# Performance work log

Hardware: AMD Instinct MI355X
Metric: run time of the kernel (lower is better)

## Reference

```python
import jax, jax.numpy as jnp
import numpy as np

N, E, F, D, H, HID, OUT, G = 25000, 400000, 128, 16, 64, 128, 32, 64

def silu(v):
    return v * jax.nn.sigmoid(v)

def setup_inputs() -> dict:
    key = jax.random.key(0)
    ks = jax.random.split(key, 32)
    inp = {
        'x': jax.random.normal(ks[0], (N, F), jnp.float32),
        'pos': jax.random.normal(ks[1], (N, 3), jnp.float32),
        'edge_attr': jax.random.normal(ks[2], (E, D), jnp.float32),
        'edge_index': jax.random.randint(ks[3], (2, E), 0, N, jnp.int64),
        'batch': jnp.sort(jax.random.randint(ks[4], (N,), 0, G, jnp.int64)),
    }
    def lin(k, fan_in, fan_out):
        return jax.random.normal(k, (fan_in, fan_out), jnp.float32) / np.sqrt(fan_in)
    i = 5
    for l, in_c in enumerate([F, HID]):
        cat = 2 * in_c + D + 1
        inp[f'l{l}_mlp_w'] = lin(ks[i], cat, H); i += 1
        inp[f'l{l}_edge_w'] = lin(ks[i], H, H); i += 1
        inp[f'l{l}_edge_b'] = jnp.zeros((H,), jnp.float32)
        inp[f'l{l}_coord_w'] = lin(ks[i], H, 1); i += 1
        inp[f'l{l}_coord_b'] = jnp.zeros((1,), jnp.float32)
        inp[f'l{l}_node_w1'] = lin(ks[i], in_c + H, H); i += 1
        inp[f'l{l}_node_b1'] = jnp.zeros((H,), jnp.float32)
        inp[f'l{l}_node_w2'] = lin(ks[i], H, HID); i += 1
        inp[f'l{l}_node_b2'] = jnp.zeros((HID,), jnp.float32)
    inp['out_w1'] = lin(ks[i], HID, HID); i += 1
    inp['out_b1'] = jnp.zeros((HID,), jnp.float32)
    inp['out_w2'] = lin(ks[i], HID, OUT); i += 1
    inp['out_b2'] = jnp.zeros((OUT,), jnp.float32)
    return inp

def egnn_layer(x, pos, src, dst, edge_attr, mlp_w, edge_w, edge_b, coord_w, coord_b, nw1, nb1, nw2, nb2):
    # PyG flow source_to_target: i = dst (edge_index[1]), j = src (edge_index[0])
    diff = pos[dst] - pos[src]                    # (E,3)
    radial = jnp.sum(diff * diff, axis=1, keepdims=True)  # (E,1)
    cat = jnp.concatenate([x[dst], x[src], edge_attr, radial], axis=1)
    h = silu(cat @ mlp_w)                         # (E,H)
    e_ij = silu(h @ edge_w + edge_b)              # (E,H)
    coord_update = diff * silu(e_ij @ coord_w + coord_b)  # (E,3)
    e_agg = jax.ops.segment_sum(e_ij, dst, num_segments=N)          # sum reduce
    cu_sum = jax.ops.segment_sum(coord_update, dst, num_segments=N)
    deg = jax.ops.segment_sum(jnp.ones((E, 1), x.dtype), dst, num_segments=N)
    cu_mean = cu_sum / jnp.maximum(deg, 1.0)      # mean reduce, 0 for isolated nodes
    h_node = silu(jnp.concatenate([x, e_agg], axis=1) @ nw1 + nb1) @ nw2 + nb2
    return h_node, pos + cu_mean

def reference(x, pos, edge_attr, edge_index, batch,
              l0_mlp_w, l0_edge_w, l0_edge_b, l0_coord_w, l0_coord_b, l0_node_w1, l0_node_b1, l0_node_w2, l0_node_b2,
              l1_mlp_w, l1_edge_w, l1_edge_b, l1_coord_w, l1_coord_b, l1_node_w1, l1_node_b1, l1_node_w2, l1_node_b2,
              out_w1, out_b1, out_w2, out_b2):
    src, dst = edge_index[0], edge_index[1]
    x, pos = egnn_layer(x, pos, src, dst, edge_attr, l0_mlp_w, l0_edge_w, l0_edge_b, l0_coord_w, l0_coord_b, l0_node_w1, l0_node_b1, l0_node_w2, l0_node_b2)
    x, pos = egnn_layer(x, pos, src, dst, edge_attr, l1_mlp_w, l1_edge_w, l1_edge_b, l1_coord_w, l1_coord_b, l1_node_w1, l1_node_b1, l1_node_w2, l1_node_b2)
    # graph mean pooling over batch assignment
    g_sum = jax.ops.segment_sum(x, batch, num_segments=G)
    g_cnt = jax.ops.segment_sum(jnp.ones((N, 1), x.dtype), batch, num_segments=G)
    g = g_sum / jnp.maximum(g_cnt, 1.0)           # (G, HID)
    g = jax.nn.relu(g)
    return jax.nn.relu(g @ out_w1 + out_b1) @ out_w2 + out_b2  # (G, OUT)
```

## Files before the change

### kernel.cpp

```cpp
#include <hip/hip_runtime.h>
#include <math.h>

#define NN 25000
#define EE 400000
#define FF 128
#define DD 16
#define HH 64
#define HIDC 128
#define OUTC 32
#define GG 64
#define NODEBLK 782
#define SCATBLK 1563
#define NTILES 1563

#define EDGEBLK 2048
#define EW_Q 3
#define EW_R 424
#define HS_STRIDE 68

#define WQ_NW1 0
#define WQ_NW2 24576
#define WQ_WN  40960
#define WQ_EW  73728
#define WQ_W3  77824
#define WQ_LAYER 81920

typedef __attribute__((ext_vector_type(8))) short short8;
typedef __attribute__((ext_vector_type(8))) unsigned short u16x8;
typedef __attribute__((ext_vector_type(4))) float f32x4;

union S8 { short8 v; unsigned short u[8]; };
union U8 { u16x8 v; unsigned short u[8]; };

__device__ __forceinline__ float silu_f(float v) {
    return v / (1.f + __expf(-v));
}

__device__ __forceinline__ unsigned short f2bf_rne(float f) {
  unsigned u = __float_as_uint(f);
  unsigned r = u + 0x7fffu + ((u >> 16) & 1u);
  return (unsigned short)(r >> 16);
}
__device__ __forceinline__ float bfbits2f(unsigned short b) {
  return __uint_as_float(((unsigned)b) << 16);
}

__device__ __forceinline__ void split8(const float* hv, S8& hi, S8& lo) {
#pragma unroll
  for (int j = 0; j < 8; ++j) {
    const unsigned short hb = (unsigned short)(__float_as_uint(hv[j]) >> 16);
    hi.u[j] = hb;
    lo.u[j] = f2bf_rne(hv[j] - bfbits2f(hb));
  }
}

__device__ __forceinline__ f32x4 mfma3(const S8& ah, const S8& al,
                                       const S8& bh, const S8& bl, f32x4 c) {
  c = __builtin_amdgcn_mfma_f32_16x16x32_bf16(ah.v, bh.v, c, 0, 0, 0);
  c = __builtin_amdgcn_mfma_f32_16x16x32_bf16(al.v, bh.v, c, 0, 0, 0);
  c = __builtin_amdgcn_mfma_f32_16x16x32_bf16(ah.v, bl.v, c, 0, 0, 0);
  return c;
}

__device__ __forceinline__ void prepSplit(unsigned short* dst, const float* __restrict__ W,
                                          int ldw, int k0, int n0, int q, int m, int lane) {
  S8 hi, lo;
#pragma unroll
  for (int j = 0; j < 8; ++j) {
    const float wv = W[(size_t)(k0 + q * 8 + j) * ldw + n0 + m];
    const unsigned short hb = (unsigned short)(__float_as_uint(wv) >> 16);
    hi.u[j] = hb;
    lo.u[j] = f2bf_rne(wv - bfbits2f(hb));
  }
  *(short8*)(dst + lane * 8) = hi.v;
  *(short8*)(dst + 512 + lane * 8) = lo.v;
}

__device__ __forceinline__ void prepB16(unsigned short* dst, const float* __restrict__ W,
                                        int ldw, int k0, int n0, int q, int m, int lane,
                                        bool zero) {
  S8 b;
#pragma unroll
  for (int j = 0; j < 8; ++j)
    b.u[j] = zero ? (unsigned short)0
                  : f2bf_rne(W[(size_t)(k0 + q * 8 + j) * ldw + n0 + m]);
  *(short8*)(dst + lane * 8) = b.v;
}

__global__ __launch_bounds__(256) void k_hist(
    const int* __restrict__ ei, int* __restrict__ cnt,
    const float* __restrict__ nw1_0, const float* __restrict__ nw2_0,
    const float* __restrict__ mlp0, const float* __restrict__ ew0,
    const float* __restrict__ nw1_1, const float* __restrict__ nw2_1,
    const float* __restrict__ mlp1, const float* __restrict__ ew1,
    unsigned short* __restrict__ wq) {
  if (blockIdx.x < SCATBLK) {
    const int t = blockIdx.x * 256 + threadIdx.x;
    if (t < EE) atomicAdd(&cnt[ei[EE + t]], 1);
    return;
  }
  const int l = blockIdx.x - SCATBLK;
  const float* nw1 = l ? nw1_1 : nw1_0;
  const float* nw2 = l ? nw2_1 : nw2_0;
  const float* mlw = l ? mlp1 : mlp0;
  const float* ew  = l ? ew1 : ew0;
  unsigned short* base = wq + (size_t)l * WQ_LAYER;
  const int tid = threadIdx.x, w = tid >> 6, lane = tid & 63;
  const int q = lane >> 4, m = lane & 15;
  for (int f = w; f < 24; f += 4)
    prepSplit(base + WQ_NW1 + f * 1024, nw1, 64, (f % 6) * 32, (f / 6) * 16, q, m, lane);
  for (int f = w; f < 16; f += 4)
    prepSplit(base + WQ_NW2 + f * 1024, nw2, 128, (f & 1) * 32, (f >> 1) * 16, q, m, lane);
  if (l == 0) {
    for (int f = w; f < 32; f += 4) {
      const int nc = f >> 2, kc = f & 3;
      prepSplit(base + WQ_WN + f * 1024, mlp1 + (size_t)(nc < 4 ? 0 : 128 * 64), 64,
                kc * 32, (nc & 3) * 16, q, m, lane);
    }
  }
  for (int f = w; f < 8; f += 4)
    prepB16(base + WQ_EW + f * 512, ew, 64, (f >> 2) * 32, (f & 3) * 16, q, m, lane, false);
  for (int f = w; f < 4; f += 4)
    prepB16(base + WQ_W3 + f * 512, mlw + 256 * 64, 64, 0, f * 16, q, m, lane, lane >= 32);
}

__global__ __launch_bounds__(1024) void k_scan(
    const int* __restrict__ cnt, int* __restrict__ row_ptr, int* __restrict__ next) {
  __shared__ int s[1024];
  const int t = threadIdx.x;
  const int base = t * 25;
  int loc[25];
  int sum = 0;
#pragma unroll
  for (int i = 0; i < 25; ++i) {
    const int n = base + i;
    loc[i] = (n < NN) ? cnt[n] : 0;
    sum += loc[i];
  }
  s[t] = sum;
  __syncthreads();
  for (int off = 1; off < 1024; off <<= 1) {
    const int v = (t >= off) ? s[t - off] : 0;
    __syncthreads();
    s[t] += v;
    __syncthreads();
  }
  int run = s[t] - sum;
#pragma unroll
  for (int i = 0; i < 25; ++i) {
    const int n = base + i;
    if (n < NN) {
      row_ptr[n] = run;
      next[n] = run;
      run += loc[i];
    }
  }
  if (t == 0) row_ptr[NN] = EE;
}

__global__ __launch_bounds__(256) void k_sp(
    const int* __restrict__ ei, int* __restrict__ next,
    int* __restrict__ sdst, int* __restrict__ ssrc, int* __restrict__ seid,
    const float* __restrict__ X, const float* __restrict__ W,
    float* __restrict__ P1, unsigned short* __restrict__ P2h) {
  __shared__ __align__(16) float xT[4][128 * 12];
  if (blockIdx.x >= NODEBLK) {
    const int t = (blockIdx.x - NODEBLK) * 256 + threadIdx.x;
    if (t < EE) {
      const int d = ei[EE + t];
      const int slot = atomicAdd(&next[d], 1);
      sdst[slot] = d;
      ssrc[slot] = ei[t];
      seid[slot] = t;
    }
    return;
  }
  const int w = threadIdx.x >> 6, lane = threadIdx.x & 63;
  float* xt = xT[w];
  const int nb = (blockIdx.x * 4 + w) * 8;
#pragma unroll
  for (int e = 0; e < 8; ++e) {
    const int n = nb + e;
    const bool v = n < NN;
    xt[lane * 12 + e]        = v ? X[n * FF + lane] : 0.f;
    xt[(lane + 64) * 12 + e] = v ? X[n * FF + 64 + lane] : 0.f;
  }
  __syncthreads();
  float a1[8], a2[8];
#pragma unroll
  for (int e = 0; e < 8; ++e) { a1[e] = 0.f; a2[e] = 0.f; }
#pragma unroll 4
  for (int k = 0; k < 128; ++k) {
    const float wa = W[k * 64 + lane];
    const float wb = W[(128 + k) * 64 + lane];
    float xk[8];
    *(f32x4*)&xk[0] = *(const f32x4*)&xt[k * 12];
    *(f32x4*)&xk[4] = *(const f32x4*)&xt[k * 12 + 4];
#pragma unroll
    for (int e = 0; e < 8; ++e) {
      a1[e] = fmaf(xk[e], wa, a1[e]);
      a2[e] = fmaf(xk[e], wb, a2[e]);
    }
  }
#pragma unroll
  for (int e = 0; e < 8; ++e) {
    const int n = nb + e;
    if (n < NN) {
      P1[n * 64 + lane]  = a1[e];
      P2h[n * 64 + lane] = f2bf_rne(a2[e]);
    }
  }
}

template <bool COORD, bool GATHER>
__global__ __launch_bounds__(256, 4) void k_edge(
    const float* __restrict__ P1, const unsigned short* __restrict__ P2h,
    const float* __restrict__ pos, const float* __restrict__ eattr,
    unsigned short* __restrict__ seattr_h, const int* __restrict__ seid,
    const int* __restrict__ sdst, const int* __restrict__ ssrc,
    const unsigned short* __restrict__ wq, const float* __restrict__ mlp_w,
    const float* __restrict__ edge_b,
    const float* __restrict__ coord_w, const float* __restrict__ coord_b,
    float* __restrict__ e_agg, float* __restrict__ cu) {
  __shared__ __align__(16) float s_hs[4][16 * HS_STRIDE];
  __shared__ float s_diff[4][48];
  __shared__ float s_rad[4][16];
  __shared__ float s_red[4][16];
  const int tid = threadIdx.x, w = tid >> 6, lane = tid & 63;
  const int q = lane >> 4, m = lane & 15;

  S8 wB[2][4];
#pragma unroll
  for (int kc = 0; kc < 2; ++kc)
#pragma unroll
    for (int nc = 0; nc < 4; ++nc)
      wB[kc][nc].v = *(const short8*)(wq + WQ_EW + (kc * 4 + nc) * 512 + lane * 8);
  S8 w3B[4];
#pragma unroll
  for (int nc = 0; nc < 4; ++nc)
    w3B[nc].v = *(const short8*)(wq + WQ_W3 + nc * 512 + lane * 8);
  float w4r[4], cwr[4], ebr[4];
#pragma unroll
  for (int nc = 0; nc < 4; ++nc) {
    w4r[nc] = mlp_w[272 * 64 + nc * 16 + m];
    ebr[nc] = edge_b[nc * 16 + m];
    cwr[nc] = COORD ? coord_w[nc * 16 + m] : 0.f;
  }
  const float cb = COORD ? coord_b[0] : 0.f;

  const int sbid = (blockIdx.x & 7) * (EDGEBLK / 8) + (blockIdx.x >> 3);
  const int wave_id = sbid * 4 + w;
  const int g0 = wave_id * EW_Q + (wave_id < EW_R ? wave_id : EW_R);
  const int ng = EW_Q + (wave_id < EW_R ? 1 : 0);

  const int pe = (lane < 48) ? (lane / 3) : 0;
  const int pc = lane - (lane / 3) * 3;

  int cur_dst = -1;
  float accum = 0.f;

  for (int g = 0; g < ng; ++g) {
    const int eb = (g0 + g) * 16;
    const int dm = sdst[eb + m];
    const int sm = ssrc[eb + m];
    f32x4 p1a[2], p1b[2];
    U8 p2r[2];
#pragma unroll
    for (int kc = 0; kc < 2; ++kc) {
      const float* pp1 = P1 + (size_t)dm * 64 + kc * 32 + q * 8;
      p1a[kc] = *(const f32x4*)pp1;
      p1b[kc] = *(const f32x4*)(pp1 + 4);
      p2r[kc].v = *(const u16x8*)(P2h + (size_t)sm * 64 + kc * 32 + q * 8);
    }
    if (lane < 48) {
      const int de = __shfl(dm, pe, 64), se = __shfl(sm, pe, 64);
      s_diff[w][lane] = pos[de * 3 + pc] - pos[se * 3 + pc];
    }
    S8 eaA;
#pragma unroll
    for (int j = 0; j < 8; ++j) eaA.u[j] = 0;
    if (lane < 32) {
      if (GATHER) {
        const int eid = seid[eb + m];
        const float* ep = &eattr[(size_t)eid * DD + q * 8];
        const f32x4 ea0 = *(const f32x4*)ep;
        const f32x4 ea1 = *(const f32x4*)(ep + 4);
#pragma unroll
        for (int j = 0; j < 4; ++j) {
          eaA.u[j]     = f2bf_rne(ea0[j]);
          eaA.u[4 + j] = f2bf_rne(ea1[j]);
        }
        *(short8*)&seattr_h[(size_t)(eb + m) * DD + q * 8] = eaA.v;
      } else {
        eaA.v = *(const short8*)&seattr_h[(size_t)(eb + m) * DD + q * 8];
      }
    }
    if (lane < 16) {
      const float d0 = s_diff[w][lane * 3 + 0];
      const float d1 = s_diff[w][lane * 3 + 1];
      const float d2 = s_diff[w][lane * 3 + 2];
      s_rad[w][lane] = fmaf(d0, d0, fmaf(d1, d1, d2 * d2));
    }
    float radr[4];
#pragma unroll
    for (int r = 0; r < 4; ++r) radr[r] = s_rad[w][q * 4 + r];
    f32x4 c3[4];
#pragma unroll
    for (int nc = 0; nc < 4; ++nc) {
      f32x4 z = {0.f, 0.f, 0.f, 0.f};
      c3[nc] = __builtin_amdgcn_mfma_f32_16x16x32_bf16(eaA.v, w3B[nc].v, z, 0, 0, 0);
    }
#pragma unroll
    for (int nc = 0; nc < 4; ++nc)
#pragma unroll
      for (int r = 0; r < 4; ++r)
        s_hs[w][(q * 4 + r) * HS_STRIDE + nc * 16 + m] = fmaf(radr[r], w4r[nc], c3[nc][r]);
    S8 ahi[2], alo[2];
#pragma unroll
    for (int kc = 0; kc < 2; ++kc) {
      const float* hp = &s_hs[w][m * HS_STRIDE + kc * 32 + q * 8];
      f32x4 h0 = *(const f32x4*)hp;
      f32x4 h1 = *(const f32x4*)(hp + 4);
      h0 = h0 + p1a[kc];
      h1 = h1 + p1b[kc];
      float hv[8];
      *(f32x4*)&hv[0] = h0;
      *(f32x4*)&hv[4] = h1;
#pragma unroll
      for (int j = 0; j < 8; ++j) {
        const float h = silu_f(hv[j] + bfbits2f(p2r[kc].u[j]));
        const unsigned short hb = (unsigned short)(__float_as_uint(h) >> 16);
        ahi[kc].u[j] = hb;
        alo[kc].u[j] = f2bf_rne(h - bfbits2f(hb));
      }
    }
    f32x4 o[4];
#pragma unroll
    for (int nc = 0; nc < 4; ++nc) {
      f32x4 bi = {ebr[nc], ebr[nc], ebr[nc], ebr[nc]};
      o[nc] = bi;
    }
#pragma unroll
    for (int kc = 0; kc < 2; ++kc)
#pragma unroll
      for (int nc = 0; nc < 4; ++nc) {
        o[nc] = __builtin_amdgcn_mfma_f32_16x16x32_bf16(ahi[kc].v, wB[kc][nc].v, o[nc], 0, 0, 0);
        o[nc] = __builtin_amdgcn_mfma_f32_16x16x32_bf16(alo[kc].v, wB[kc][nc].v, o[nc], 0, 0, 0);
      }
#pragma unroll
    for (int nc = 0; nc < 4; ++nc)
#pragma unroll
      for (int r = 0; r < 4; ++r) o[nc][r] = silu_f(o[nc][r]);
    if (COORD) {
#pragma unroll
      for (int r = 0; r < 4; ++r) {
        float v = o[0][r] * cwr[0] + o[1][r] * cwr[1] + o[2][r] * cwr[2] + o[3][r] * cwr[3];
        v += __shfl_xor(v, 1, 64);
        v += __shfl_xor(v, 2, 64);
        v += __shfl_xor(v, 4, 64);
        v += __shfl_xor(v, 8, 64);
        if (m == 0) s_red[w][q * 4 + r] = v;
      }
    }
#pragma unroll
    for (int nc = 0; nc < 4; ++nc)
#pragma unroll
      for (int r = 0; r < 4; ++r)
        s_hs[w][(q * 4 + r) * HS_STRIDE + nc * 16 + m] = o[nc][r];
    for (int e = 0; e < 16; ++e) {
      const int dv = __shfl(dm, e, 64);
      const float v = s_hs[w][e * HS_STRIDE + lane];
      if (dv == cur_dst) {
        accum += v;
      } else {
        if (cur_dst >= 0) atomicAdd(&e_agg[(size_t)cur_dst * 64 + lane], accum);
        cur_dst = dv;
        accum = v;
      }
    }
    if (COORD) {
      if (lane < 48) {
        const float s = silu_f(s_red[w][pe] + cb);
        atomicAdd(&cu[(size_t)__shfl(dm, pe, 64) * 3 + pc], s_diff[w][lane] * s);
      }
    }
  }
  if (cur_dst >= 0) atomicAdd(&e_agg[(size_t)cur_dst * 64 + lane], accum);
}

template <bool L0>
__global__ __launch_bounds__(256) void k_node(
    const float* __restrict__ x_in, float* __restrict__ e_agg,
    const unsigned short* __restrict__ wq,
    const float* __restrict__ nb1, const float* __restrict__ nb2,
    const float* __restrict__ pos_in, const float* __restrict__ cu,
    const int* __restrict__ row_ptr,
    float* __restrict__ x_out, float* __restrict__ pos_out,
    float* __restrict__ P1, unsigned short* __restrict__ P2h,
    const int* __restrict__ batch,
    float* __restrict__ g_sum, float* __restrict__ g_cnt) {
  __shared__ __align__(16) float sb[16 * 132];
  const int tid = threadIdx.x, w = tid >> 6, lane = tid & 63;
  const int q = lane >> 4, m = lane & 15;
  const int n0 = blockIdx.x * 16;
  const int nm = n0 + m;
  const bool vm = nm < NN;

  S8 axh[6], axl[6];
#pragma unroll
  for (int kc = 0; kc < 6; ++kc) {
    float hv[8] = {0.f, 0.f, 0.f, 0.f, 0.f, 0.f, 0.f, 0.f};
    if (vm) {
      const float* src = (kc < 4) ? (x_in + (size_t)nm * HIDC + kc * 32 + q * 8)
                                  : (e_agg + (size_t)nm * 64 + (kc - 4) * 32 + q * 8);
      *(f32x4*)&hv[0] = *(const f32x4*)src;
      *(f32x4*)&hv[4] = *(const f32x4*)(src + 4);
    }
    split8(hv, axh[kc], axl[kc]);
  }
  {
    const float b = nb1[w * 16 + m];
    f32x4 acc = {b, b, b, b};
#pragma unroll
    for (int kc = 0; kc < 6; ++kc) {
      S8 bh, bl;
      const unsigned short* fb = wq + WQ_NW1 + (w * 6 + kc) * 1024 + lane * 8;
      bh.v = *(const short8*)fb;
      bl.v = *(const short8*)(fb + 512);
      acc = mfma3(axh[kc], axl[kc], bh, bl, acc);
    }
#pragma unroll
    for (int r = 0; r < 4; ++r)
      sb[(q * 4 + r) * 132 + w * 16 + m] = silu_f(acc[r]);
  }
  __syncthreads();
  if (L0 && vm && w == 3) {
    const f32x4 z = {0.f, 0.f, 0.f, 0.f};
    float* ez = e_agg + (size_t)nm * 64 + q * 8;
    *(f32x4*)ez = z; *(f32x4*)(ez + 4) = z;
    *(f32x4*)(ez + 32) = z; *(f32x4*)(ez + 36) = z;
  }
  S8 ah[2], al[2];
#pragma unroll
  for (int kc = 0; kc < 2; ++kc) {
    float hv[8];
    const float* hp = &sb[m * 132 + kc * 32 + q * 8];
    *(f32x4*)&hv[0] = *(const f32x4*)hp;
    *(f32x4*)&hv[4] = *(const f32x4*)(hp + 4);
    split8(hv, ah[kc], al[kc]);
  }
  f32x4 hh[2];
#pragma unroll
  for (int i = 0; i < 2; ++i) {
    const int nc = w + i * 4;
    const float b = nb2[nc * 16 + m];
    f32x4 acc = {b, b, b, b};
#pragma unroll
    for (int kc = 0; kc < 2; ++kc) {
      S8 bh, bl;
      const unsigned short* fb = wq + WQ_NW2 + (nc * 2 + kc) * 1024 + lane * 8;
      bh.v = *(const short8*)fb;
      bl.v = *(const short8*)(fb + 512);
      acc = mfma3(ah[kc], al[kc], bh, bl, acc);
    }
    hh[i] = acc;
  }
  if (L0) {
    __syncthreads();
#pragma unroll
    for (int i = 0; i < 2; ++i) {
      const int nc = w + i * 4;
#pragma unroll
      for (int r = 0; r < 4; ++r) {
        const int n = n0 + q * 4 + r;
        sb[(q * 4 + r) * 132 + nc * 16 + m] = hh[i][r];
        if (n < NN) x_out[(size_t)n * HIDC + nc * 16 + m] = hh[i][r];
      }
    }
    if (w == 0 && lane < 48) {
      const int pe2 = lane / 3, pc2 = lane - pe2 * 3;
      const int n = n0 + pe2;
      if (n < NN) {
        const float dg = fmaxf((float)(row_ptr[n + 1] - row_ptr[n]), 1.f);
        pos_out[n * 3 + pc2] = pos_in[n * 3 + pc2] + cu[n * 3 + pc2] / dg;
      }
    }
    __syncthreads();
    S8 a1h[4], a1l[4];
#pragma unroll
    for (int kc = 0; kc < 4; ++kc) {
      float hv[8];
      const float* hp = &sb[m * 132 + kc * 32 + q * 8];
      *(f32x4*)&hv[0] = *(const f32x4*)hp;
      *(f32x4*)&hv[4] = *(const f32x4*)(hp + 4);
      split8(hv, a1h[kc], a1l[kc]);
    }
#pragma unroll
    for (int i = 0; i < 2; ++i) {
      const int nc = w + i * 4;
      f32x4 acc = {0.f, 0.f, 0.f, 0.f};
#pragma unroll
      for (int kc = 0; kc < 4; ++kc) {
        S8 bh, bl;
        const unsigned short* fb = wq + WQ_WN + (nc * 4 + kc) * 1024 + lane * 8;
        bh.v = *(const short8*)fb;
        bl.v = *(const short8*)(fb + 512);
        acc = mfma3(a1h[kc], a1l[kc], bh, bl, acc);
      }
#pragma unroll
      for (int r = 0; r < 4; ++r) {
        const int n = n0 + q * 4 + r;
        if (n < NN) {
          if (i == 0) P1[(size_t)n * 64 + w * 16 + m] = acc[r];
          else        P2h[(size_t)n * 64 + w * 16 + m] = f2bf_rne(acc[r]);
        }
      }
    }
  } else {
    int curb = -1;
    float cnt2 = 0.f;
    float pacc[2];
#pragma unroll
    for (int r = 0; r < 4; ++r) {
      const int n = n0 + q * 4 + r;
      if (n < NN) {
        const int bg = batch[n];
        if (bg != curb) {
          if (curb >= 0) {
#pragma unroll
            for (int i = 0; i < 2; ++i)
              atomicAdd(&g_sum[curb * HIDC + (w + i * 4) * 16 + m], pacc[i]);
            if (w == 0 && m == 0) atomicAdd(&g_cnt[curb], cnt2);
          }
          curb = bg;
          pacc[0] = hh[0][r];
          pacc[1] = hh[1][r];
          cnt2 = 1.f;
        } else {
          pacc[0] += hh[0][r];
          pacc[1] += hh[1][r];
          cnt2 += 1.f;
        }
      }
    }
    if (curb >= 0) {
#pragma unroll
      for (int i = 0; i < 2; ++i)
        atomicAdd(&g_sum[curb * HIDC + (w + i * 4) * 16 + m], pacc[i]);
      if (w == 0 && m == 0) atomicAdd(&g_cnt[curb], cnt2);
    }
  }
}

__global__ __launch_bounds__(128) void k_final(
    const float* __restrict__ g_sum, const float* __restrict__ g_cnt,
    const float* __restrict__ w1, const float* __restrict__ b1,
    const float* __restrict__ w2, const float* __restrict__ b2,
    float* __restrict__ out) {
  __shared__ float sg[128];
  __shared__ float sh[128];
  const int g = blockIdx.x, j = threadIdx.x;
  const float c = fmaxf(g_cnt[g], 1.f);
  sg[j] = fmaxf(g_sum[g * HIDC + j] / c, 0.f);
  __syncthreads();
  float a = b1[j];
  for (int k = 0; k < 128; ++k) a += sg[k] * w1[k * 128 + j];
  sh[j] = fmaxf(a, 0.f);
  __syncthreads();
  if (j < OUTC) {
    float o = b2[j];
    for (int k = 0; k < 128; ++k) o += sh[k] * w2[k * OUTC + j];
    out[g * OUTC + j] = o;
  }
}

extern "C" void kernel_launch(void* const* d_in, const int* in_sizes, int n_in,
                              void* d_out, int out_size, void* d_ws, size_t ws_size,
                              hipStream_t stream) {
  const float* x     = (const float*)d_in[0];
  const float* pos   = (const float*)d_in[1];
  const float* eattr = (const float*)d_in[2];
  const int*   ei    = (const int*)d_in[3];
  const int*   batch = (const int*)d_in[4];
  const float* mlp_w[2]   = {(const float*)d_in[5],  (const float*)d_in[14]};
  const float* edge_w[2]  = {(const float*)d_in[6],  (const float*)d_in[15]};
  const float* edge_b[2]  = {(const float*)d_in[7],  (const float*)d_in[16]};
  const float* coord_w[2] = {(const float*)d_in[8],  (const float*)d_in[17]};
  const float* coord_b[2] = {(const float*)d_in[9],  (const float*)d_in[18]};
  const float* nw1[2]     = {(const float*)d_in[10], (const float*)d_in[19]};
  const float* nb1[2]     = {(const float*)d_in[11], (const float*)d_in[20]};
  const float* nw2[2]     = {(const float*)d_in[12], (const float*)d_in[21]};
  const float* nb2[2]     = {(const float*)d_in[13], (const float*)d_in[22]};
  const float* ow1 = (const float*)d_in[23];
  const float* ob1 = (const float*)d_in[24];
  const float* ow2 = (const float*)d_in[25];
  const float* ob2 = (const float*)d_in[26];
  float* out = (float*)d_out;

  char* p = (char*)d_ws;
  auto alloc = [&](size_t bytes) {
    void* r = (void*)p;
    p += (bytes + 255) & ~(size_t)255;
    return r;
  };
  float* P1            = (float*)alloc((size_t)NN * 64 * 4);
  unsigned short* P2h  = (unsigned short*)alloc((size_t)NN * 64 * 2);
  char* zero_base      = p;
  float* e_agg         = (float*)alloc((size_t)NN * 64 * 4);
  float* cu            = (float*)alloc((size_t)NN * 3 * 4);
  float* g_sum         = (float*)alloc((size_t)GG * HIDC * 4);
  float* g_cnt         = (float*)alloc((size_t)GG * 4);
  int* cnt             = (int*)alloc((size_t)NN * 4);
  const size_t zero_sz = (size_t)(p - zero_base);
  int* row_ptr         = (int*)alloc((size_t)(NN + 1) * 4);
  int* nxt             = (int*)alloc((size_t)NN * 4);
  int* sdst            = (int*)alloc((size_t)EE * 4);
  int* ssrc            = (int*)alloc((size_t)EE * 4);
  int* seid            = (int*)alloc((size_t)EE * 4);
  unsigned short* seah = (unsigned short*)alloc((size_t)EE * DD * 2);
  float* x1            = (float*)alloc((size_t)NN * HIDC * 4);
  float* pos1          = (float*)alloc((size_t)NN * 3 * 4);
  unsigned short* wqb  = (unsigned short*)alloc((size_t)2 * WQ_LAYER * 2);

  (void)hipMemsetAsync(zero_base, 0, zero_sz, stream);

  k_hist<<<SCATBLK + 2, 256, 0, stream>>>(ei, cnt,
      nw1[0], nw2[0], mlp_w[0], edge_w[0],
      nw1[1], nw2[1], mlp_w[1], edge_w[1], wqb);
  k_scan<<<1, 1024, 0, stream>>>(cnt, row_ptr, nxt);
  k_sp<<<NODEBLK + SCATBLK, 256, 0, stream>>>(ei, nxt, sdst, ssrc, seid,
      x, mlp_w[0], P1, P2h);

  k_edge<true, true><<<EDGEBLK, 256, 0, stream>>>(P1, P2h, pos, eattr,
      seah, seid, sdst, ssrc, wqb, mlp_w[0], edge_b[0],
      coord_w[0], coord_b[0], e_agg, cu);
  k_node<true><<<NTILES, 256, 0, stream>>>(x, e_agg, wqb, nb1[0], nb2[0],
      pos, cu, row_ptr, x1, pos1, P1, P2h, batch, g_sum, g_cnt);

  k_edge<false, false><<<EDGEBLK, 256, 0, stream>>>(P1, P2h, pos1, eattr,
      seah, seid, sdst, ssrc, wqb + WQ_LAYER, mlp_w[1], edge_b[1],
      coord_w[1], coord_b[1], e_agg, cu);
  k_node<false><<<NTILES, 256, 0, stream>>>(x1, e_agg, wqb + WQ_LAYER,
      nb1[1], nb2[1], pos1, cu, row_ptr, x1, pos1, P1, P2h,
      batch, g_sum, g_cnt);

  k_final<<<GG, 128, 0, stream>>>(g_sum, g_cnt, ow1, ob1, ow2, ob2, out);
}
```

Before: 458.8 us.

## Software-pipeline edge kernel gathers with double-buffered register prefetch

```diff
diff --git a/kernel.cpp b/kernel.cpp
--- a/kernel.cpp
+++ b/kernel.cpp
@@ -13,9 +13,9 @@
 #define SCATBLK 1563
 #define NTILES 1563
 
-#define EDGEBLK 2048
+#define EDGEBLK 1792
 #define EW_Q 3
-#define EW_R 424
+#define EW_R 3496
 #define HS_STRIDE 68
 
 #define WQ_NW1 0
@@ -213,7 +213,7 @@
 }
 
 template <bool COORD, bool GATHER>
-__global__ __launch_bounds__(256, 4) void k_edge(
+__global__ __launch_bounds__(256, 3) void k_edge(
     const float* __restrict__ P1, const unsigned short* __restrict__ P2h,
     const float* __restrict__ pos, const float* __restrict__ eattr,
     unsigned short* __restrict__ seattr_h, const int* __restrict__ seid,
@@ -248,143 +248,177 @@
   }
   const float cb = COORD ? coord_b[0] : 0.f;
 
-  const int sbid = (blockIdx.x & 7) * (EDGEBLK / 8) + (blockIdx.x >> 3);
-  const int wave_id = sbid * 4 + w;
+  const int wave_id = blockIdx.x * 4 + w;
   const int g0 = wave_id * EW_Q + (wave_id < EW_R ? wave_id : EW_R);
   const int ng = EW_Q + (wave_id < EW_R ? 1 : 0);
 
   const int pe = (lane < 48) ? (lane / 3) : 0;
   const int pc = lane - (lane / 3) * 3;
 
+  int dmv[4], smv[4], eiv[4];
+#pragma unroll
+  for (int i = 0; i < 4; ++i) {
+    const int eb = (g0 + ((i < 3) ? i : (ng - 1))) * 16;
+    dmv[i] = sdst[eb + m];
+    smv[i] = ssrc[eb + m];
+    eiv[i] = GATHER ? seid[eb + m] : 0;
+  }
+
+  f32x4 Pa[2][2], Pb[2][2];
+  U8 Pr[2][2];
+  f32x4 E0[2], E1[2];
+  U8 Eh[2];
+  float Pdd[2], Pss[2];
+
+#define PREF(i, s) do {                                                        \
+    const int dm_ = dmv[i], sm_ = smv[i];                                      \
+    const float* pp_ = P1 + (size_t)dm_ * 64 + q * 8;                          \
+    Pa[s][0] = *(const f32x4*)pp_;                                             \
+    Pb[s][0] = *(const f32x4*)(pp_ + 4);                                       \
+    Pa[s][1] = *(const f32x4*)(pp_ + 32);                                      \
+    Pb[s][1] = *(const f32x4*)(pp_ + 36);                                      \
+    const unsigned short* pr_ = P2h + (size_t)sm_ * 64 + q * 8;                \
+    Pr[s][0].v = *(const u16x8*)pr_;                                           \
+    Pr[s][1].v = *(const u16x8*)(pr_ + 32);                                    \
+    const int de_ = __shfl(dm_, pe, 64), se_ = __shfl(sm_, pe, 64);            \
+    if (lane < 48) { Pdd[s] = pos[de_ * 3 + pc]; Pss[s] = pos[se_ * 3 + pc]; } \
+    if (lane < 32) {                                                           \
+      if (GATHER) {                                                            \
+        const float* ep_ = &eattr[(size_t)eiv[i] * DD + q * 8];                \
+        E0[s] = *(const f32x4*)ep_;                                            \
+        E1[s] = *(const f32x4*)(ep_ + 4);                                      \
+      } else {                                                                 \
+        Eh[s].v = *(const u16x8*)&seattr_h[(size_t)((g0 + (i)) * 16 + m) * DD + q * 8]; \
+      }                                                                        \
+    }                                                                          \
+  } while (0)
+
+#define COMPUTE(g, s) do {                                                     \
+    const int eb_ = (g0 + (g)) * 16;                                           \
+    const int dm_ = dmv[g];                                                    \
+    if (lane < 48) s_diff[w][lane] = Pdd[s] - Pss[s];                          \
+    S8 eaA_;                                                                   \
+    _Pragma("unroll")                                                          \
+    for (int j_ = 0; j_ < 8; ++j_) eaA_.u[j_] = 0;                             \
+    if (lane < 32) {                                                           \
+      if (GATHER) {                                                            \
+        _Pragma("unroll")                                                      \
+        for (int j_ = 0; j_ < 4; ++j_) {                                       \
+          eaA_.u[j_]     = f2bf_rne(E0[s][j_]);                                \
+          eaA_.u[4 + j_] = f2bf_rne(E1[s][j_]);                                \
+        }                                                                      \
+        *(short8*)&seattr_h[(size_t)(eb_ + m) * DD + q * 8] = eaA_.v;          \
+      } else {                                                                 \
+        eaA_.v = *(const short8*)&Eh[s];                                       \
+      }                                                                        \
+    }                                                                          \
+    if (lane < 16) {                                                           \
+      const float d0_ = s_diff[w][lane * 3 + 0];                               \
+      const float d1_ = s_diff[w][lane * 3 + 1];                               \
+      const float d2_ = s_diff[w][lane * 3 + 2];                               \
+      s_rad[w][lane] = fmaf(d0_, d0_, fmaf(d1_, d1_, d2_ * d2_));              \
+    }                                                                          \
+    float radr_[4];                                                            \
+    _Pragma("unroll")                                                          \
+    for (int r_ = 0; r_ < 4; ++r_) radr_[r_] = s_rad[w][q * 4 + r_];           \
+    f32x4 c3_[4];                                                              \
+    _Pragma("unroll")                                                          \
+    for (int nc_ = 0; nc_ < 4; ++nc_) {                                        \
+      f32x4 z_ = {0.f, 0.f, 0.f, 0.f};                                         \
+      c3_[nc_] = __builtin_amdgcn_mfma_f32_16x16x32_bf16(eaA_.v, w3B[nc_].v, z_, 0, 0, 0); \
+    }                                                                          \
+    _Pragma("unroll")                                                          \
+    for (int nc_ = 0; nc_ < 4; ++nc_)                                          \
+      _Pragma("unroll")                                                        \
+      for (int r_ = 0; r_ < 4; ++r_)                                           \
+        s_hs[w][(q * 4 + r_) * HS_STRIDE + nc_ * 16 + m] =                     \
+            fmaf(radr_[r_], w4r[nc_], c3_[nc_][r_]);                           \
+    S8 ahi_[2], alo_[2];                                                       \
+    _Pragma("unroll")                                                          \
+    for (int kc_ = 0; kc_ < 2; ++kc_) {                                        \
+      const float* hp_ = &s_hs[w][m * HS_STRIDE + kc_ * 32 + q * 8];           \
+      f32x4 h0_ = *(const f32x4*)hp_;                                          \
+      f32x4 h1_ = *(const f32x4*)(hp_ + 4);                                    \
+      h0_ = h0_ + Pa[s][kc_];                                                  \
+      h1_ = h1_ + Pb[s][kc_];                                                  \
+      float hv_[8];                                                            \
+      *(f32x4*)&hv_[0] = h0_;                                                  \
+      *(f32x4*)&hv_[4] = h1_;                                                  \
+      _Pragma("unroll")                                                        \
+      for (int j_ = 0; j_ < 8; ++j_) {                                         \
+        const float h_ = silu_f(hv_[j_] + bfbits2f(Pr[s][kc_].u[j_]));         \
+        const unsigned short hb_ = (unsigned short)(__float_as_uint(h_) >> 16);\
+        ahi_[kc_].u[j_] = hb_;                                                 \
+        alo_[kc_].u[j_] = f2bf_rne(h_ - bfbits2f(hb_));                        \
+      }                                                                        \
+    }                                                                          \
+    f32x4 o_[4];                                                               \
+    _Pragma("unroll")                                                          \
+    for (int nc_ = 0; nc_ < 4; ++nc_) {                                        \
+      f32x4 bi_ = {ebr[nc_], ebr[nc_], ebr[nc_], ebr[nc_]};                    \
+      o_[nc_] = bi_;                                                           \
+    }                                                                          \
+    _Pragma("unroll")                                                          \
+    for (int kc_ = 0; kc_ < 2; ++kc_)                                          \
+      _Pragma("unroll")                                                        \
+      for (int nc_ = 0; nc_ < 4; ++nc_) {                                      \
+        o_[nc_] = __builtin_amdgcn_mfma_f32_16x16x32_bf16(ahi_[kc_].v, wB[kc_][nc_].v, o_[nc_], 0, 0, 0); \
+        o_[nc_] = __builtin_amdgcn_mfma_f32_16x16x32_bf16(alo_[kc_].v, wB[kc_][nc_].v, o_[nc_], 0, 0, 0); \
+      }                                                                        \
+    _Pragma("unroll")                                                          \
+    for (int nc_ = 0; nc_ < 4; ++nc_)                                          \
+      _Pragma("unroll")                                                        \
+      for (int r_ = 0; r_ < 4; ++r_) o_[nc_][r_] = silu_f(o_[nc_][r_]);        \
+    if (COORD) {                                                               \
+      _Pragma("unroll")                                                        \
+      for (int r_ = 0; r_ < 4; ++r_) {                                         \
+        float v_ = o_[0][r_] * cwr[0] + o_[1][r_] * cwr[1] + o_[2][r_] * cwr[2] + o_[3][r_] * cwr[3]; \
+        v_ += __shfl_xor(v_, 1, 64);                                           \
+        v_ += __shfl_xor(v_, 2, 64);                                           \
+        v_ += __shfl_xor(v_, 4, 64);                                           \
+        v_ += __shfl_xor(v_, 8, 64);                                           \
+        if (m == 0) s_red[w][q * 4 + r_] = v_;                                 \
+      }                                                                        \
+    }                                                                          \
+    _Pragma("unroll")                                                          \
+    for (int nc_ = 0; nc_ < 4; ++nc_)                                          \
+      _Pragma("unroll")                                                        \
+      for (int r_ = 0; r_ < 4; ++r_)                                           \
+        s_hs[w][(q * 4 + r_) * HS_STRIDE + nc_ * 16 + m] = o_[nc_][r_];        \
+    for (int e_ = 0; e_ < 16; ++e_) {                                          \
+      const int dv_ = __shfl(dm_, e_, 64);                                     \
+      const float v_ = s_hs[w][e_ * HS_STRIDE + lane];                         \
+      if (dv_ == cur_dst) {                                                    \
+        accum += v_;                                                           \
+      } else {                                                                 \
+        if (cur_dst >= 0) atomicAdd(&e_agg[(size_t)cur_dst * 64 + lane], accum); \
+        cur_dst = dv_;                                                         \
+        accum = v_;                                                            \
+      }                                                                        \
+    }                                                                          \
+    if (COORD) {                                                               \
+      if (lane < 48) {                                                         \
+        const float sc_ = silu_f(s_red[w][pe] + cb);                           \
+        atomicAdd(&cu[(size_t)__shfl(dm_, pe, 64) * 3 + pc], s_diff[w][lane] * sc_); \
+      }                                                                        \
+    }                                                                          \
+  } while (0)
+
   int cur_dst = -1;
   float accum = 0.f;
 
-  for (int g = 0; g < ng; ++g) {
-    const int eb = (g0 + g) * 16;
-    const int dm = sdst[eb + m];
-    const int sm = ssrc[eb + m];
-    f32x4 p1a[2], p1b[2];
-    U8 p2r[2];
-#pragma unroll
-    for (int kc = 0; kc < 2; ++kc) {
-      const float* pp1 = P1 + (size_t)dm * 64 + kc * 32 + q * 8;
-      p1a[kc] = *(const f32x4*)pp1;
-      p1b[kc] = *(const f32x4*)(pp1 + 4);
-      p2r[kc].v = *(const u16x8*)(P2h + (size_t)sm * 64 + kc * 32 + q * 8);
-    }
-    if (lane < 48) {
-      const int de = __shfl(dm, pe, 64), se = __shfl(sm, pe, 64);
-      s_diff[w][lane] = pos[de * 3 + pc] - pos[se * 3 + pc];
-    }
-    S8 eaA;
-#pragma unroll
-    for (int j = 0; j < 8; ++j) eaA.u[j] = 0;
-    if (lane < 32) {
-      if (GATHER) {
-        const int eid = seid[eb + m];
-        const float* ep = &eattr[(size_t)eid * DD + q * 8];
-        const f32x4 ea0 = *(const f32x4*)ep;
-        const f32x4 ea1 = *(const f32x4*)(ep + 4);
-#pragma unroll
-        for (int j = 0; j < 4; ++j) {
-          eaA.u[j]     = f2bf_rne(ea0[j]);
-          eaA.u[4 + j] = f2bf_rne(ea1[j]);
-        }
-        *(short8*)&seattr_h[(size_t)(eb + m) * DD + q * 8] = eaA.v;
-      } else {
-        eaA.v = *(const short8*)&seattr_h[(size_t)(eb + m) * DD + q * 8];
-      }
-    }
-    if (lane < 16) {
-      const float d0 = s_diff[w][lane * 3 + 0];
-      const float d1 = s_diff[w][lane * 3 + 1];
-      const float d2 = s_diff[w][lane * 3 + 2];
-      s_rad[w][lane] = fmaf(d0, d0, fmaf(d1, d1, d2 * d2));
-    }
-    float radr[4];
-#pragma unroll
-    for (int r = 0; r < 4; ++r) radr[r] = s_rad[w][q * 4 + r];
-    f32x4 c3[4];
-#pragma unroll
-    for (int nc = 0; nc < 4; ++nc) {
-      f32x4 z = {0.f, 0.f, 0.f, 0.f};
-      c3[nc] = __builtin_amdgcn_mfma_f32_16x16x32_bf16(eaA.v, w3B[nc].v, z, 0, 0, 0);
-    }
-#pragma unroll
-    for (int nc = 0; nc < 4; ++nc)
-#pragma unroll
-      for (int r = 0; r < 4; ++r)
-        s_hs[w][(q * 4 + r) * HS_STRIDE + nc * 16 + m] = fmaf(radr[r], w4r[nc], c3[nc][r]);
-    S8 ahi[2], alo[2];
-#pragma unroll
-    for (int kc = 0; kc < 2; ++kc) {
-      const float* hp = &s_hs[w][m * HS_STRIDE + kc * 32 + q * 8];
-      f32x4 h0 = *(const f32x4*)hp;
-      f32x4 h1 = *(const f32x4*)(hp + 4);
-      h0 = h0 + p1a[kc];
-      h1 = h1 + p1b[kc];
-      float hv[8];
-      *(f32x4*)&hv[0] = h0;
-      *(f32x4*)&hv[4] = h1;
-#pragma unroll
-      for (int j = 0; j < 8; ++j) {
-        const float h = silu_f(hv[j] + bfbits2f(p2r[kc].u[j]));
-        const unsigned short hb = (unsigned short)(__float_as_uint(h) >> 16);
-        ahi[kc].u[j] = hb;
-        alo[kc].u[j] = f2bf_rne(h - bfbits2f(hb));
-      }
-    }
-    f32x4 o[4];
-#pragma unroll
-    for (int nc = 0; nc < 4; ++nc) {
-      f32x4 bi = {ebr[nc], ebr[nc], ebr[nc], ebr[nc]};
-      o[nc] = bi;
-    }
-#pragma unroll
-    for (int kc = 0; kc < 2; ++kc)
-#pragma unroll
-      for (int nc = 0; nc < 4; ++nc) {
-        o[nc] = __builtin_amdgcn_mfma_f32_16x16x32_bf16(ahi[kc].v, wB[kc][nc].v, o[nc], 0, 0, 0);
-        o[nc] = __builtin_amdgcn_mfma_f32_16x16x32_bf16(alo[kc].v, wB[kc][nc].v, o[nc], 0, 0, 0);
-      }
-#pragma unroll
-    for (int nc = 0; nc < 4; ++nc)
-#pragma unroll
-      for (int r = 0; r < 4; ++r) o[nc][r] = silu_f(o[nc][r]);
-    if (COORD) {
-#pragma unroll
-      for (int r = 0; r < 4; ++r) {
-        float v = o[0][r] * cwr[0] + o[1][r] * cwr[1] + o[2][r] * cwr[2] + o[3][r] * cwr[3];
-        v += __shfl_xor(v, 1, 64);
-        v += __shfl_xor(v, 2, 64);
-        v += __shfl_xor(v, 4, 64);
-        v += __shfl_xor(v, 8, 64);
-        if (m == 0) s_red[w][q * 4 + r] = v;
-      }
-    }
-#pragma unroll
-    for (int nc = 0; nc < 4; ++nc)
-#pragma unroll
-      for (int r = 0; r < 4; ++r)
-        s_hs[w][(q * 4 + r) * HS_STRIDE + nc * 16 + m] = o[nc][r];
-    for (int e = 0; e < 16; ++e) {
-      const int dv = __shfl(dm, e, 64);
-      const float v = s_hs[w][e * HS_STRIDE + lane];
-      if (dv == cur_dst) {
-        accum += v;
-      } else {
-        if (cur_dst >= 0) atomicAdd(&e_agg[(size_t)cur_dst * 64 + lane], accum);
-        cur_dst = dv;
-        accum = v;
-      }
-    }
-    if (COORD) {
-      if (lane < 48) {
-        const float s = silu_f(s_red[w][pe] + cb);
-        atomicAdd(&cu[(size_t)__shfl(dm, pe, 64) * 3 + pc], s_diff[w][lane] * s);
-      }
-    }
-  }
+  PREF(0, 0);
+  PREF(1, 1);
+  COMPUTE(0, 0);
+  PREF(2, 0);
+  COMPUTE(1, 1);
+  if (ng == 4) PREF(3, 1);
+  COMPUTE(2, 0);
+  if (ng == 4) COMPUTE(3, 1);
+
+#undef PREF
+#undef COMPUTE
+
   if (cur_dst >= 0) atomicAdd(&e_agg[(size_t)cur_dst * 64 + lane], accum);
 }
 
```

After: 497.8 us. +8.5%, slower.

## Pack sorted edge records with bf16 attributes during scatter; rebalance edge grid

Applied to the files above, without the earlier changes.

```diff
diff --git a/kernel.cpp b/kernel.cpp
--- a/kernel.cpp
+++ b/kernel.cpp
@@ -13,10 +13,11 @@
 #define SCATBLK 1563
 #define NTILES 1563
 
-#define EDGEBLK 2048
+#define EDGEBLK 1792
 #define EW_Q 3
-#define EW_R 424
+#define EW_R 3496
 #define HS_STRIDE 68
+#define RECB 48
 
 #define WQ_NW1 0
 #define WQ_NW2 24576
@@ -160,7 +161,7 @@
 
 __global__ __launch_bounds__(256) void k_sp(
     const int* __restrict__ ei, int* __restrict__ next,
-    int* __restrict__ sdst, int* __restrict__ ssrc, int* __restrict__ seid,
+    char* __restrict__ rec, const float* __restrict__ eattr,
     const float* __restrict__ X, const float* __restrict__ W,
     float* __restrict__ P1, unsigned short* __restrict__ P2h) {
   __shared__ __align__(16) float xT[4][128 * 12];
@@ -168,10 +169,20 @@
     const int t = (blockIdx.x - NODEBLK) * 256 + threadIdx.x;
     if (t < EE) {
       const int d = ei[EE + t];
+      const int s = ei[t];
       const int slot = atomicAdd(&next[d], 1);
-      sdst[slot] = d;
-      ssrc[slot] = ei[t];
-      seid[slot] = t;
+      const float* ep = &eattr[(size_t)t * DD];
+      S8 a0, a1;
+#pragma unroll
+      for (int j = 0; j < 8; ++j) {
+        a0.u[j] = f2bf_rne(ep[j]);
+        a1.u[j] = f2bf_rne(ep[8 + j]);
+      }
+      char* rp = rec + (size_t)slot * RECB;
+      int hdr[4] = {d, s, 0, 0};
+      *(f32x4*)rp = *(const f32x4*)hdr;
+      *(short8*)(rp + 16) = a0.v;
+      *(short8*)(rp + 32) = a1.v;
     }
     return;
   }
@@ -212,12 +223,10 @@
   }
 }
 
-template <bool COORD, bool GATHER>
+template <bool COORD>
 __global__ __launch_bounds__(256, 4) void k_edge(
     const float* __restrict__ P1, const unsigned short* __restrict__ P2h,
-    const float* __restrict__ pos, const float* __restrict__ eattr,
-    unsigned short* __restrict__ seattr_h, const int* __restrict__ seid,
-    const int* __restrict__ sdst, const int* __restrict__ ssrc,
+    const float* __restrict__ pos, const char* __restrict__ rec,
     const unsigned short* __restrict__ wq, const float* __restrict__ mlp_w,
     const float* __restrict__ edge_b,
     const float* __restrict__ coord_w, const float* __restrict__ coord_b,
@@ -248,8 +257,7 @@
   }
   const float cb = COORD ? coord_b[0] : 0.f;
 
-  const int sbid = (blockIdx.x & 7) * (EDGEBLK / 8) + (blockIdx.x >> 3);
-  const int wave_id = sbid * 4 + w;
+  const int wave_id = blockIdx.x * 4 + w;
   const int g0 = wave_id * EW_Q + (wave_id < EW_R ? wave_id : EW_R);
   const int ng = EW_Q + (wave_id < EW_R ? 1 : 0);
 
@@ -261,8 +269,9 @@
 
   for (int g = 0; g < ng; ++g) {
     const int eb = (g0 + g) * 16;
-    const int dm = sdst[eb + m];
-    const int sm = ssrc[eb + m];
+    const char* rp = rec + (size_t)(eb + m) * RECB;
+    const int dm = ((const int*)rp)[0];
+    const int sm = ((const int*)rp)[1];
     f32x4 p1a[2], p1b[2];
     U8 p2r[2];
 #pragma unroll
@@ -280,20 +289,7 @@
 #pragma unroll
     for (int j = 0; j < 8; ++j) eaA.u[j] = 0;
     if (lane < 32) {
-      if (GATHER) {
-        const int eid = seid[eb + m];
-        const float* ep = &eattr[(size_t)eid * DD + q * 8];
-        const f32x4 ea0 = *(const f32x4*)ep;
-        const f32x4 ea1 = *(const f32x4*)(ep + 4);
-#pragma unroll
-        for (int j = 0; j < 4; ++j) {
-          eaA.u[j]     = f2bf_rne(ea0[j]);
-          eaA.u[4 + j] = f2bf_rne(ea1[j]);
-        }
-        *(short8*)&seattr_h[(size_t)(eb + m) * DD + q * 8] = eaA.v;
-      } else {
-        eaA.v = *(const short8*)&seattr_h[(size_t)(eb + m) * DD + q * 8];
-      }
+      eaA.v = *(const short8*)(rp + 16 + q * 16);
     }
     if (lane < 16) {
       const float d0 = s_diff[w][lane * 3 + 0];
@@ -614,10 +610,7 @@
   const size_t zero_sz = (size_t)(p - zero_base);
   int* row_ptr         = (int*)alloc((size_t)(NN + 1) * 4);
   int* nxt             = (int*)alloc((size_t)NN * 4);
-  int* sdst            = (int*)alloc((size_t)EE * 4);
-  int* ssrc            = (int*)alloc((size_t)EE * 4);
-  int* seid            = (int*)alloc((size_t)EE * 4);
-  unsigned short* seah = (unsigned short*)alloc((size_t)EE * DD * 2);
+  char* rec            = (char*)alloc((size_t)EE * RECB);
   float* x1            = (float*)alloc((size_t)NN * HIDC * 4);
   float* pos1          = (float*)alloc((size_t)NN * 3 * 4);
   unsigned short* wqb  = (unsigned short*)alloc((size_t)2 * WQ_LAYER * 2);
@@ -628,18 +621,16 @@
       nw1[0], nw2[0], mlp_w[0], edge_w[0],
       nw1[1], nw2[1], mlp_w[1], edge_w[1], wqb);
   k_scan<<<1, 1024, 0, stream>>>(cnt, row_ptr, nxt);
-  k_sp<<<NODEBLK + SCATBLK, 256, 0, stream>>>(ei, nxt, sdst, ssrc, seid,
+  k_sp<<<NODEBLK + SCATBLK, 256, 0, stream>>>(ei, nxt, rec, eattr,
       x, mlp_w[0], P1, P2h);
 
-  k_edge<true, true><<<EDGEBLK, 256, 0, stream>>>(P1, P2h, pos, eattr,
-      seah, seid, sdst, ssrc, wqb, mlp_w[0], edge_b[0],
-      coord_w[0], coord_b[0], e_agg, cu);
+  k_edge<true><<<EDGEBLK, 256, 0, stream>>>(P1, P2h, pos, rec,
+      wqb, mlp_w[0], edge_b[0], coord_w[0], coord_b[0], e_agg, cu);
   k_node<true><<<NTILES, 256, 0, stream>>>(x, e_agg, wqb, nb1[0], nb2[0],
       pos, cu, row_ptr, x1, pos1, P1, P2h, batch, g_sum, g_cnt);
 
-  k_edge<false, false><<<EDGEBLK, 256, 0, stream>>>(P1, P2h, pos1, eattr,
-      seah, seid, sdst, ssrc, wqb + WQ_LAYER, mlp_w[1], edge_b[1],
-      coord_w[1], coord_b[1], e_agg, cu);
+  k_edge<false><<<EDGEBLK, 256, 0, stream>>>(P1, P2h, pos1, rec,
+      wqb + WQ_LAYER, mlp_w[1], edge_b[1], coord_w[1], coord_b[1], e_agg, cu);
   k_node<false><<<NTILES, 256, 0, stream>>>(x1, e_agg, wqb + WQ_LAYER,
       nb1[1], nb2[1], pos1, cu, row_ptr, x1, pos1, P1, P2h,
       batch, g_sum, g_cnt);
```

After: 446.4 us. 1.03x faster.
